# Optimization experiments

Measured on AMD Instinct MI355X. Metric: run time of the kernel, lower is better.

## Reference

```python
import jax, jax.numpy as jnp
import numpy as np

B, T, D, W, H = 64, 512, 768, 255, 8
DH = D // H

def layernorm(x, g, b, eps=1e-5):
    m = jnp.mean(x, axis=-1, keepdims=True)
    v = jnp.mean((x - m) ** 2, axis=-1, keepdims=True)
    return (x - m) * jax.lax.rsqrt(v + eps) * g + b

def setup_inputs() -> dict:
    key = jax.random.key(0)
    ks = list(jax.random.split(key, 12))
    p = lambda k, shape, s=0.02: (jax.random.normal(k, shape, jnp.float32) * s)
    # words_ids: -100 at CLS/SEP, each word spans 2 subtokens -> 255 words/row
    wi = np.full((B, T), -100, dtype=np.int32)
    pos = np.arange(1, T - 1)
    wi[:, 1:T - 1] = (pos - 1) // 2
    return {
        'output_bert': jax.random.normal(ks[0], (B, T, D), jnp.float32),
        'words_ids': jnp.asarray(wi),
        'Wq': p(ks[1], (D, D)), 'bq': jnp.zeros((D,), jnp.float32),
        'Wk': p(ks[2], (D, D)), 'bk': jnp.zeros((D,), jnp.float32),
        'Wv': p(ks[3], (D, D)), 'bv': jnp.zeros((D,), jnp.float32),
        'Wo': p(ks[4], (D, D)), 'bo': jnp.zeros((D,), jnp.float32),
        'ln1_g': jnp.ones((D,), jnp.float32), 'ln1_b': jnp.zeros((D,), jnp.float32),
        'W1f': p(ks[5], (D, 4 * D)), 'b1f': jnp.zeros((4 * D,), jnp.float32),
        'W2f': p(ks[6], (4 * D, D)), 'b2f': jnp.zeros((D,), jnp.float32),
        'ln2_g': jnp.ones((D,), jnp.float32), 'ln2_b': jnp.zeros((D,), jnp.float32),
        'ng': jnp.ones((D,), jnp.float32), 'nb': jnp.zeros((D,), jnp.float32),
        'lin_w': p(ks[7], (D, 2)), 'lin_b': jnp.zeros((2,), jnp.float32),
    }

def reference(output_bert, words_ids, Wq, bq, Wk, bk, Wv, bv, Wo, bo,
              ln1_g, ln1_b, W1f, b1f, W2f, b2f, ln2_g, ln2_b, ng, nb, lin_w, lin_b):
    Bsz = output_bert.shape[0]
    # --- first-subtoken gather: first token position of each word id ---
    hits = words_ids[:, None, :] == jnp.arange(W)[None, :, None]   # [B, W, T]
    first_idx = jnp.argmax(hits, axis=-1)                           # [B, W]
    feat = jnp.take_along_axis(output_bert, first_idx[..., None], axis=1)  # [B, W, D]
    # --- transformer encoder layer (post-norm, relu FFN) ---
    q = (feat @ Wq + bq).reshape(Bsz, W, H, DH)
    k = (feat @ Wk + bk).reshape(Bsz, W, H, DH)
    v = (feat @ Wv + bv).reshape(Bsz, W, H, DH)
    scores = jnp.einsum('bqhd,bkhd->bhqk', q, k) * (1.0 / np.sqrt(DH))
    attn = jax.nn.softmax(scores, axis=-1)
    ctx = jnp.einsum('bhqk,bkhd->bqhd', attn, v).reshape(Bsz, W, D)
    x = layernorm(feat + ctx @ Wo + bo, ln1_g, ln1_b)
    ff = jax.nn.relu(x @ W1f + b1f) @ W2f + b2f
    x = layernorm(x + ff, ln2_g, ln2_b)
    # --- final LayerNorm + Linear + softmax + argmax path ---
    x = layernorm(x, ng, nb)
    logits = x @ lin_w + lin_b
    ner_prob = jax.nn.softmax(logits, axis=-1)
    path = jnp.argmax(ner_prob, axis=-1)
    return ner_prob, path
```

## Files before the change

### kernel.cpp

```cpp
#include <hip/hip_runtime.h>
#include <cmath>

#define Bsz 64
#define Tt  512
#define Dd  768
#define Wn  255
#define Hh  8
#define DHd 96
#define NROWS (Bsz*Wn)

typedef _Float16 half_t;
typedef _Float16 f16x8 __attribute__((ext_vector_type(8)));
typedef _Float16 f16x4 __attribute__((ext_vector_type(4)));
typedef float f32x4 __attribute__((ext_vector_type(4)));

#define OFF_QKV_H 0
#define OFF_QKV_L 1769472
#define OFF_WO_H 3538944
#define OFF_WO_L 4128768
#define OFF_W1_H 4718592
#define OFF_W1_L 7077888
#define OFF_W2_H 9437184
#define OFF_W2_L 11796480
#define SLOTH 25165824
__device__ __align__(16) half_t g_w16[14155776];

__device__ __forceinline__ void gload16(const half_t* g, half_t* l) {
    __builtin_amdgcn_global_load_lds((const __attribute__((address_space(1))) void*)g,
                                     (__attribute__((address_space(3))) void*)l, 16, 0, 0);
}


__global__ void k_init_fi(int* fi) {
    int i = blockIdx.x * 256 + threadIdx.x;
    if (i < Bsz * Wn) fi[i] = 0x7fffffff;
}

__global__ void k_scan(const int* __restrict__ wid, int* __restrict__ fi) {
    int i = blockIdx.x * 256 + threadIdx.x;
    if (i >= Bsz * Tt) return;
    int b = i / Tt, t = i % Tt;
    int w = wid[i];
    if (w >= 0 && w < Wn) atomicMin(&fi[b * Wn + w], t);
}

__global__ void k_bcat(const float* __restrict__ bq, const float* __restrict__ bk,
                       const float* __restrict__ bv, float* __restrict__ o) {
    int i = blockIdx.x * 256 + threadIdx.x;
    if (i < 768) o[i] = bq[i];
    else if (i < 1536) o[i] = bk[i - 768];
    else if (i < 2304) o[i] = bv[i - 1536];
}

__global__ void k_gather(const float4* __restrict__ ob, const int* __restrict__ fi,
                         half_t* __restrict__ f16) {
    int i = blockIdx.x * 256 + threadIdx.x;
    if (i >= NROWS * 192) return;
    int r = i / 192, c = i % 192;
    int b = r / Wn;
    int idx = fi[r];
    if (idx == 0x7fffffff) idx = 0;
    float4 v = ob[((size_t)b * Tt + idx) * 192 + c];
    float a0 = v.x * 16.f, a1 = v.y * 16.f, a2 = v.z * 16.f, a3 = v.w * 16.f;
    half_t h0 = (half_t)a0, h1 = (half_t)a1, h2 = (half_t)a2, h3 = (half_t)a3;
    f16x4 hv = {h0, h1, h2, h3};
    f16x4 lv = {(half_t)(a0 - (float)h0), (half_t)(a1 - (float)h1),
                (half_t)(a2 - (float)h2), (half_t)(a3 - (float)h3)};
    size_t off = (size_t)r * 1536 + c * 4;
    *(f16x4*)&f16[off] = hv;
    *(f16x4*)&f16[off + 768] = lv;
}


__global__ void k_wsplit(const float* __restrict__ Wm, int K, int N,
                         size_t off_h, size_t off_l) {
    __shared__ float sm[32][33];
    const int tx = threadIdx.x, ty = threadIdx.y;
    const int n0 = blockIdx.x * 32, k0 = blockIdx.y * 32;
    #pragma unroll
    for (int r = 0; r < 4; ++r)
        sm[ty + r * 8][tx] = Wm[(size_t)(k0 + ty + r * 8) * N + n0 + tx];
    __syncthreads();
    half_t* oh = g_w16 + off_h;
    half_t* ol = g_w16 + off_l;
    #pragma unroll
    for (int r = 0; r < 4; ++r) {
        float v = 64.f * sm[tx][ty + r * 8];
        half_t hi = (half_t)v;
        size_t o = (size_t)(n0 + ty + r * 8) * K + k0 + tx;
        oh[o] = hi;
        ol[o] = (half_t)(v - (float)hi);
    }
}


template<int MODE, int AMODE, int NTILE>
__global__ __launch_bounds__(256, NTILE == 64 ? 3 : 2) void k_gemm16(
    const half_t* __restrict__ Ah, const half_t* __restrict__ Al, int lda,
    size_t boff_h, size_t boff_l,
    const float* __restrict__ bias,
    const void* __restrict__ res,
    void* __restrict__ out0, void* __restrict__ out1,
    int M, int N, int K) {
    constexpr int MI = (NTILE == 128 ? 4 : 2);
    __shared__ half_t sA[2][128 * 32];
    __shared__ half_t sB[2][NTILE * 32];
    const int tid = threadIdx.x;
    const int w = tid >> 6, l = tid & 63;
    int lin = blockIdx.y * gridDim.x + blockIdx.x;
    int rpx = gridDim.y >> 3;
    int j_ = lin >> 3;
    int jr = j_ / gridDim.x;
    int by = (lin & 7) * rpx + jr;
    int bx = j_ - jr * gridDim.x;
    const int row0 = by * 128, col0 = bx * NTILE;
    const half_t* Bh = g_w16 + boff_h;
    const half_t* Bl = g_w16 + boff_l;

    const int srow = l >> 2;
    const int skk  = (l & 3) * 8;
    const int fr = l & 15, qk = (l >> 4) * 8;
    const int mh = (NTILE == 128) ? (w >> 1) * 64 : w * 32;
    const int nh = (NTILE == 128) ? (w & 1) * 64 : 0;

    f32x4 acc[MI][4];
    #pragma unroll
    for (int i = 0; i < MI; ++i)
        #pragma unroll
        for (int j = 0; j < 4; ++j) acc[i][j] = (f32x4){0.f, 0.f, 0.f, 0.f};

    for (int k0 = 0; k0 < K; k0 += 32) {
        #pragma unroll
        for (int t = 0; t < 2; ++t) {
            int r = (w * 2 + t) * 16 + srow;
            int grA = row0 + r; if (grA >= M) grA = M - 1;
            half_t* da  = (half_t*)&sA[0][(w * 2 + t) * 512];
            half_t* da2 = (half_t*)&sA[1][(w * 2 + t) * 512];
            if (AMODE == 1) {
                int b = grA / 255, wl = grA - b * 255;
                int kk = k0 + skk;
                int h = kk / 96, d = kk - h * 96;
                size_t aoff = ((size_t)(b * 8 + h) * 256 + wl) * 192 + d;
                gload16(Ah + aoff, da);
                gload16(Al + aoff, da2);
            } else {
                gload16(Ah + (size_t)grA * lda + k0 + skk, da);
                gload16(Al + (size_t)grA * lda + k0 + skk, da2);
            }
            if (NTILE == 128 || t == 0) {
                int bs = (NTILE == 128) ? (w * 2 + t) : w;
                int grB = col0 + bs * 16 + srow;
                gload16(Bh + (size_t)grB * K + k0 + skk, (half_t*)&sB[0][bs * 512]);
                gload16(Bl + (size_t)grB * K + k0 + skk, (half_t*)&sB[1][bs * 512]);
            }
        }
        __syncthreads();
        f16x8 a0[MI], a1[MI], b0[4], b1[4];
        #pragma unroll
        for (int i = 0; i < MI; ++i) {
            a0[i] = *(const f16x8*)&sA[0][(mh + i * 16 + fr) * 32 + qk];
            a1[i] = *(const f16x8*)&sA[1][(mh + i * 16 + fr) * 32 + qk];
        }
        #pragma unroll
        for (int j = 0; j < 4; ++j) {
            b0[j] = *(const f16x8*)&sB[0][(nh + j * 16 + fr) * 32 + qk];
            b1[j] = *(const f16x8*)&sB[1][(nh + j * 16 + fr) * 32 + qk];
        }
        #pragma unroll
        for (int i = 0; i < MI; ++i)
            #pragma unroll
            for (int j = 0; j < 4; ++j) {
                acc[i][j] = __builtin_amdgcn_mfma_f32_16x16x32_f16(a0[i], b0[j], acc[i][j], 0, 0, 0);
                acc[i][j] = __builtin_amdgcn_mfma_f32_16x16x32_f16(a0[i], b1[j], acc[i][j], 0, 0, 0);
                acc[i][j] = __builtin_amdgcn_mfma_f32_16x16x32_f16(a1[i], b0[j], acc[i][j], 0, 0, 0);
            }
        __syncthreads();
    }

    const float dsc = 1.0f / 1024.0f;
    #pragma unroll
    for (int i = 0; i < MI; ++i) {
        #pragma unroll
        for (int r = 0; r < 4; ++r) {
            int row = row0 + mh + i * 16 + ((l >> 4) << 2) + r;
            if (row >= M) continue;
            #pragma unroll
            for (int j = 0; j < 4; ++j) {
                int col = col0 + nh + j * 16 + (l & 15);
                float vv = acc[i][j][r] * dsc + bias[col];
                if (MODE == 5) {
                    int b = row / 255, wl = row - b * 255;
                    int part = col / 768;
                    int cc = col - part * 768;
                    int h = cc / 96, d = cc - h * 96;
                    float t16 = vv * 16.f;
                    half_t hi = (half_t)t16;
                    half_t lo = (half_t)(t16 - (float)hi);
                    half_t* dst = (half_t*)out0 + (size_t)part * SLOTH;
                    size_t o = ((size_t)(b * 8 + h) * 256 + wl) * 192 + d;
                    dst[o] = hi; dst[o + 96] = lo;
                } else if (MODE == 1) {
                    const half_t* rp = (const half_t*)res;
                    vv += ((float)rp[(size_t)row * 1536 + col] +
                           (float)rp[(size_t)row * 1536 + 768 + col]) * 0.0625f;
                    ((float*)out0)[(size_t)row * N + col] = vv;
                } else if (MODE == 2) {
                    vv = fmaxf(vv, 0.f);
                    float t16 = vv * 16.f;
                    half_t hi = (half_t)t16;
                    ((half_t*)out0)[(size_t)row * N + col] = hi;
                    ((half_t*)out1)[(size_t)row * N + col] = (half_t)(t16 - (float)hi);
                } else {
                    vv += ((const float*)res)[(size_t)row * N + col];
                    ((float*)out0)[(size_t)row * N + col] = vv;
                }
            }
        }
    }
}


__global__ __launch_bounds__(256, 2) void k_attn2(half_t* __restrict__ qc,
                                                  const half_t* __restrict__ kk16,
                                                  const half_t* __restrict__ vv16) {
    __shared__ half_t sK[64][200];
    __shared__ half_t sVT[192][72];
    __shared__ float  sP[4][16][68];
    const int tid = threadIdx.x;
    const int w = tid >> 6, l = tid & 63;
    const int lr = l & 15, lc = l >> 4;
    const size_t base = (size_t)blockIdx.x * 49152;
    const float ssc = 0.10206207261596575f / 256.0f;

    for (int pass = 0; pass < 2; ++pass) {
        f32x4 O[2][6];
        float mrow[2][4], lrow[2][4];
        #pragma unroll
        for (int qs = 0; qs < 2; ++qs) {
            #pragma unroll
            for (int dn = 0; dn < 6; ++dn) O[qs][dn] = (f32x4){0.f, 0.f, 0.f, 0.f};
            #pragma unroll
            for (int r = 0; r < 4; ++r) { mrow[qs][r] = -3e38f; lrow[qs][r] = 0.f; }
        }
        for (int kt = 0; kt < 4; ++kt) {
            __syncthreads();
            #pragma unroll
            for (int c = 0; c < 6; ++c) {
                int ch = w + c * 4;
                *(f16x8*)&sK[l][ch * 8] =
                    *(const f16x8*)(kk16 + base + (size_t)(kt * 64 + l) * 192 + ch * 8);
            }
            #pragma unroll
            for (int c = 0; c < 6; ++c) {
                int ch = w + c * 4;
                f16x8 vv = *(const f16x8*)(vv16 + base + (size_t)(kt * 64 + l) * 192 + ch * 8);
                #pragma unroll
                for (int j = 0; j < 8; ++j) sVT[ch * 8 + j][l] = vv[j];
            }
            __syncthreads();
            #pragma unroll
            for (int qs = 0; qs < 2; ++qs) {
                const int qrow0 = (pass * 2 + qs) * 64 + w * 16;
                f16x8 qf0[3], qf1[3];
                #pragma unroll
                for (int s = 0; s < 3; ++s) {
                    qf0[s] = *(const f16x8*)(qc + base + (size_t)(qrow0 + lr) * 192 + s * 32 + lc * 8);
                    qf1[s] = *(const f16x8*)(qc + base + (size_t)(qrow0 + lr) * 192 + 96 + s * 32 + lc * 8);
                }
                f32x4 sacc[4];
                #pragma unroll
                for (int nt = 0; nt < 4; ++nt) sacc[nt] = (f32x4){0.f, 0.f, 0.f, 0.f};
                #pragma unroll
                for (int s = 0; s < 3; ++s)
                    #pragma unroll
                    for (int nt = 0; nt < 4; ++nt) {
                        f16x8 kh = *(const f16x8*)&sK[nt * 16 + lr][s * 32 + lc * 8];
                        f16x8 klo = *(const f16x8*)&sK[nt * 16 + lr][96 + s * 32 + lc * 8];
                        sacc[nt] = __builtin_amdgcn_mfma_f32_16x16x32_f16(qf0[s], kh, sacc[nt], 0, 0, 0);
                        sacc[nt] = __builtin_amdgcn_mfma_f32_16x16x32_f16(qf0[s], klo, sacc[nt], 0, 0, 0);
                        sacc[nt] = __builtin_amdgcn_mfma_f32_16x16x32_f16(qf1[s], kh, sacc[nt], 0, 0, 0);
                    }
                float sv[4][4], mx[4] = {-3e38f, -3e38f, -3e38f, -3e38f};
                #pragma unroll
                for (int nt = 0; nt < 4; ++nt) {
                    int key = kt * 64 + nt * 16 + lr;
                    #pragma unroll
                    for (int r = 0; r < 4; ++r) {
                        float s_ = sacc[nt][r] * ssc;
                        if (key >= 255) s_ = -3e38f;
                        sv[nt][r] = s_;
                        mx[r] = fmaxf(mx[r], s_);
                    }
                }
                #pragma unroll
                for (int r = 0; r < 4; ++r) {
                    mx[r] = fmaxf(mx[r], __shfl_xor(mx[r], 1));
                    mx[r] = fmaxf(mx[r], __shfl_xor(mx[r], 2));
                    mx[r] = fmaxf(mx[r], __shfl_xor(mx[r], 4));
                    mx[r] = fmaxf(mx[r], __shfl_xor(mx[r], 8));
                }
                float alpha[4], rsum[4];
                #pragma unroll
                for (int r = 0; r < 4; ++r) {
                    float mn = fmaxf(mrow[qs][r], mx[r]);
                    alpha[r] = __expf(mrow[qs][r] - mn);
                    mrow[qs][r] = mn;
                    rsum[r] = 0.f;
                }
                float pv[4][4];
                #pragma unroll
                for (int nt = 0; nt < 4; ++nt)
                    #pragma unroll
                    for (int r = 0; r < 4; ++r) {
                        float p = __expf(sv[nt][r] - mrow[qs][r]);
                        pv[nt][r] = p;
                        rsum[r] += p;
                    }
                #pragma unroll
                for (int r = 0; r < 4; ++r) {
                    rsum[r] += __shfl_xor(rsum[r], 1);
                    rsum[r] += __shfl_xor(rsum[r], 2);
                    rsum[r] += __shfl_xor(rsum[r], 4);
                    rsum[r] += __shfl_xor(rsum[r], 8);
                    lrow[qs][r] = lrow[qs][r] * alpha[r] + rsum[r];
                }
                #pragma unroll
                for (int dn = 0; dn < 6; ++dn)
                    #pragma unroll
                    for (int r = 0; r < 4; ++r) O[qs][dn][r] *= alpha[r];
                #pragma unroll
                for (int nt = 0; nt < 4; ++nt)
                    #pragma unroll
                    for (int r = 0; r < 4; ++r)
                        sP[w][lc * 4 + r][nt * 16 + lr] = pv[nt][r];
                #pragma unroll
                for (int ks = 0; ks < 2; ++ks) {
                    const float* pp = &sP[w][lr][ks * 32 + lc * 8];
                    f16x8 ph, pl;
                    #pragma unroll
                    for (int j = 0; j < 8; ++j) {
                        float p = pp[j];
                        half_t h_ = (half_t)p;
                        ph[j] = h_;
                        pl[j] = (half_t)(p - (float)h_);
                    }
                    #pragma unroll
                    for (int dn = 0; dn < 6; ++dn) {
                        f16x8 vh = *(const f16x8*)&sVT[dn * 16 + lr][ks * 32 + lc * 8];
                        f16x8 vl = *(const f16x8*)&sVT[96 + dn * 16 + lr][ks * 32 + lc * 8];
                        O[qs][dn] = __builtin_amdgcn_mfma_f32_16x16x32_f16(ph, vh, O[qs][dn], 0, 0, 0);
                        O[qs][dn] = __builtin_amdgcn_mfma_f32_16x16x32_f16(ph, vl, O[qs][dn], 0, 0, 0);
                        O[qs][dn] = __builtin_amdgcn_mfma_f32_16x16x32_f16(pl, vh, O[qs][dn], 0, 0, 0);
                    }
                }
            }
        }
        #pragma unroll
        for (int qs = 0; qs < 2; ++qs) {
            const int qrow0 = (pass * 2 + qs) * 64 + w * 16;
            #pragma unroll
            for (int r = 0; r < 4; ++r) {
                int qrow = qrow0 + lc * 4 + r;
                if (qrow >= Wn) continue;
                float inv = 1.0f / lrow[qs][r];
                #pragma unroll
                for (int dn = 0; dn < 6; ++dn) {
                    float val = O[qs][dn][r] * inv;
                    half_t hi = (half_t)val;
                    half_t lo = (half_t)(val - (float)hi);
                    size_t o = base + (size_t)qrow * 192 + dn * 16 + lr;
                    qc[o] = hi;
                    qc[o + 96] = lo;
                }
            }
        }
    }
}


template<int SPLIT>
__global__ __launch_bounds__(256) void k_ln(const float* __restrict__ X, const float* __restrict__ g,
                                            const float* __restrict__ bt, float* __restrict__ Y,
                                            half_t* __restrict__ Y16) {
    const int r = blockIdx.x, tid = threadIdx.x;
    __shared__ float red[256];
    const float* x = X + (size_t)r * Dd;
    float x0 = x[tid], x1 = x[tid + 256], x2 = x[tid + 512];
    red[tid] = x0 + x1 + x2; __syncthreads();
    for (int s = 128; s > 0; s >>= 1) { if (tid < s) red[tid] += red[tid + s]; __syncthreads(); }
    float mean = red[0] * (1.0f / 768.0f);
    __syncthreads();
    float d0 = x0 - mean, d1 = x1 - mean, d2 = x2 - mean;
    red[tid] = d0 * d0 + d1 * d1 + d2 * d2; __syncthreads();
    for (int s = 128; s > 0; s >>= 1) { if (tid < s) red[tid] += red[tid + s]; __syncthreads(); }
    float rs = rsqrtf(red[0] * (1.0f / 768.0f) + 1e-5f);
    float* y = Y + (size_t)r * Dd;
    float y0 = d0 * rs * g[tid]       + bt[tid];
    float y1 = d1 * rs * g[tid + 256] + bt[tid + 256];
    float y2 = d2 * rs * g[tid + 512] + bt[tid + 512];
    y[tid] = y0; y[tid + 256] = y1; y[tid + 512] = y2;
    if (SPLIT) {
        half_t* h = Y16 + (size_t)r * 1536;
        float t0 = y0 * 16.f, t1 = y1 * 16.f, t2 = y2 * 16.f;
        half_t h0 = (half_t)t0, h1 = (half_t)t1, h2 = (half_t)t2;
        h[tid] = h0; h[tid + 256] = h1; h[tid + 512] = h2;
        h[768 + tid] = (half_t)(t0 - (float)h0);
        h[768 + tid + 256] = (half_t)(t1 - (float)h1);
        h[768 + tid + 512] = (half_t)(t2 - (float)h2);
    }
}


__global__ __launch_bounds__(256) void k_final(const float* __restrict__ X, const float* __restrict__ g,
                                               const float* __restrict__ bt, const float* __restrict__ lw,
                                               const float* __restrict__ lb, float* __restrict__ out) {
    const int r = blockIdx.x, tid = threadIdx.x;
    __shared__ float red[256];
    const float* x = X + (size_t)r * Dd;
    float x0 = x[tid], x1 = x[tid + 256], x2 = x[tid + 512];
    red[tid] = x0 + x1 + x2; __syncthreads();
    for (int s = 128; s > 0; s >>= 1) { if (tid < s) red[tid] += red[tid + s]; __syncthreads(); }
    float mean = red[0] * (1.0f / 768.0f);
    __syncthreads();
    float d0 = x0 - mean, d1 = x1 - mean, d2 = x2 - mean;
    red[tid] = d0 * d0 + d1 * d1 + d2 * d2; __syncthreads();
    for (int s = 128; s > 0; s >>= 1) { if (tid < s) red[tid] += red[tid + s]; __syncthreads(); }
    float rs = rsqrtf(red[0] * (1.0f / 768.0f) + 1e-5f);
    __syncthreads();
    float n0 = d0 * rs * g[tid]       + bt[tid];
    float n1 = d1 * rs * g[tid + 256] + bt[tid + 256];
    float n2 = d2 * rs * g[tid + 512] + bt[tid + 512];
    float l0 = n0 * lw[2 * tid]     + n1 * lw[2 * (tid + 256)]     + n2 * lw[2 * (tid + 512)];
    float l1 = n0 * lw[2 * tid + 1] + n1 * lw[2 * (tid + 256) + 1] + n2 * lw[2 * (tid + 512) + 1];
    red[tid] = l0; __syncthreads();
    for (int s = 128; s > 0; s >>= 1) { if (tid < s) red[tid] += red[tid + s]; __syncthreads(); }
    l0 = red[0]; __syncthreads();
    red[tid] = l1; __syncthreads();
    for (int s = 128; s > 0; s >>= 1) { if (tid < s) red[tid] += red[tid + s]; __syncthreads(); }
    l1 = red[0];
    if (tid == 0) {
        l0 += lb[0]; l1 += lb[1];
        float m = fmaxf(l0, l1);
        float e0 = expf(l0 - m), e1 = expf(l1 - m);
        float inv = 1.0f / (e0 + e1);
        out[2 * r] = e0 * inv;
        out[2 * r + 1] = e1 * inv;
        out[2 * NROWS + r] = (l1 > l0) ? 1.0f : 0.0f;
    }
}


extern "C" void kernel_launch(void* const* d_in, const int* in_sizes, int n_in,
                              void* d_out, int out_size, void* d_ws, size_t ws_size,
                              hipStream_t stream) {
    const float* ob  = (const float*)d_in[0];
    const int*   wid = (const int*)d_in[1];
    const float* Wq  = (const float*)d_in[2];  const float* bq  = (const float*)d_in[3];
    const float* Wk  = (const float*)d_in[4];  const float* bk  = (const float*)d_in[5];
    const float* Wv  = (const float*)d_in[6];  const float* bv  = (const float*)d_in[7];
    const float* Wo  = (const float*)d_in[8];  const float* bo  = (const float*)d_in[9];
    const float* g1  = (const float*)d_in[10]; const float* b1  = (const float*)d_in[11];
    const float* W1f = (const float*)d_in[12]; const float* b1f = (const float*)d_in[13];
    const float* W2f = (const float*)d_in[14]; const float* b2f = (const float*)d_in[15];
    const float* g2  = (const float*)d_in[16]; const float* b2  = (const float*)d_in[17];
    const float* ng  = (const float*)d_in[18]; const float* nb  = (const float*)d_in[19];
    const float* lw  = (const float*)d_in[20]; const float* lb  = (const float*)d_in[21];
    float* out = (float*)d_out;

    char* ws = (char*)d_ws;
    const size_t MB = 1u << 20;
    const size_t SLOT = 48 * MB;
    int* fi = (int*)ws;
    float* bcat = (float*)(ws + 262144);
    char* S1 = ws + MB;
    char* S2 = S1 + SLOT;
    char* S3 = S2 + SLOT;
    char* S4 = S3 + SLOT;

    half_t* feat16 = (half_t*)S1;
    half_t* q16    = (half_t*)S2;
    half_t* k16    = (half_t*)S3;
    half_t* v16    = (half_t*)S4;
    float*  t1     = (float*)S3;
    float*  xbuf   = (float*)S4;
    half_t* x16    = (half_t*)S2;
    half_t* ffh_h  = (half_t*)S1;
    half_t* ffh_l  = (half_t*)S3;
    float*  t2     = (float*)S2;
    float*  x2     = (float*)S4;

    k_wsplit<<<dim3(24, 24), dim3(32, 8), 0, stream>>>(Wq, 768, 768, 0, 1769472);
    k_wsplit<<<dim3(24, 24), dim3(32, 8), 0, stream>>>(Wk, 768, 768, 589824, 2359296);
    k_wsplit<<<dim3(24, 24), dim3(32, 8), 0, stream>>>(Wv, 768, 768, 1179648, 2949120);
    k_wsplit<<<dim3(24, 24), dim3(32, 8), 0, stream>>>(Wo, 768, 768, OFF_WO_H, OFF_WO_L);
    k_wsplit<<<dim3(96, 24), dim3(32, 8), 0, stream>>>(W1f, 768, 3072, OFF_W1_H, OFF_W1_L);
    k_wsplit<<<dim3(24, 96), dim3(32, 8), 0, stream>>>(W2f, 3072, 768, OFF_W2_H, OFF_W2_L);
    k_bcat<<<9, 256, 0, stream>>>(bq, bk, bv, bcat);

    k_init_fi<<<(Bsz * Wn + 255) / 256, 256, 0, stream>>>(fi);
    k_scan<<<(Bsz * Tt) / 256, 256, 0, stream>>>(wid, fi);
    k_gather<<<(NROWS * 192 + 255) / 256, 256, 0, stream>>>((const float4*)ob, fi, feat16);

    k_gemm16<5, 0, 128><<<dim3(18, 128), 256, 0, stream>>>(
        feat16, feat16 + 768, 1536, OFF_QKV_H, OFF_QKV_L,
        bcat, nullptr, q16, nullptr, NROWS, 2304, Dd);

    k_attn2<<<Bsz * Hh, 256, 0, stream>>>(q16, k16, v16);

    k_gemm16<1, 1, 128><<<dim3(6, 128), 256, 0, stream>>>(
        q16, q16 + 96, 0, OFF_WO_H, OFF_WO_L,
        bo, feat16, t1, nullptr, NROWS, Dd, Dd);
    k_ln<1><<<NROWS, 256, 0, stream>>>(t1, g1, b1, xbuf, x16);

    for (int c = 0; c < 2; ++c) {
        const int r0 = c * 8160, mc = 8160;
        k_gemm16<2, 0, 128><<<dim3(24, 64), 256, 0, stream>>>(
            x16 + (size_t)r0 * 1536, x16 + (size_t)r0 * 1536 + 768, 1536,
            OFF_W1_H, OFF_W1_L, b1f, nullptr, ffh_h, ffh_l, mc, 3072, Dd);
        k_gemm16<3, 0, 64><<<dim3(12, 64), 256, 0, stream>>>(
            ffh_h, ffh_l, 3072, OFF_W2_H, OFF_W2_L, b2f, xbuf + (size_t)r0 * Dd,
            t2 + (size_t)r0 * Dd, nullptr, mc, Dd, 3072);
    }

    k_ln<0><<<NROWS, 256, 0, stream>>>(t2, g2, b2, x2, nullptr);
    k_final<<<NROWS, 256, 0, stream>>>(x2, ng, nb, lw, lb, out);
}
```

Baseline: 1.144 ms.

## Replace split-fp16 GEMMs with 256x256 pipelined kernel over concatenated K segments

Replaces the 128-wide double-buffered GEMM with a 512-thread 256x256 tile kernel. The split-precision hi/lo products become one long K loop over a pre-concatenated [hi|hi|lo] weight layout, so each iteration issues two MFMAs instead of three separate accumulations. The kernel uses XOR-swizzled LDS, split-phase prefetch with explicit vmcnt waits, and s_setprio around MFMA bursts. The FFN is restructured into three hidden-dimension chunks whose W2 outputs accumulate in place into xbuf. This targets larger data reuse and better overlap of loads with compute, but it raises register pressure and leaves partial tiles for M=16320 and N=768.

```diff
diff --git a/kernel.cpp b/kernel.cpp
--- a/kernel.cpp
+++ b/kernel.cpp
@@ -14,16 +14,12 @@
 typedef _Float16 f16x4 __attribute__((ext_vector_type(4)));
 typedef float f32x4 __attribute__((ext_vector_type(4)));
 
-#define OFF_QKV_H 0
-#define OFF_QKV_L 1769472
-#define OFF_WO_H 3538944
-#define OFF_WO_L 4128768
-#define OFF_W1_H 4718592
-#define OFF_W1_L 7077888
-#define OFF_W2_H 9437184
-#define OFF_W2_L 11796480
+#define OFF_QKV 0
+#define OFF_WO  5308416
+#define OFF_W1  7077888
+#define OFF_W2  14155776
 #define SLOTH 25165824
-__device__ __align__(16) half_t g_w16[14155776];
+__device__ __align__(16) half_t g_w16[21233664];
 
 __device__ __forceinline__ void gload16(const half_t* g, half_t* l) {
     __builtin_amdgcn_global_load_lds((const __attribute__((address_space(1))) void*)g,
@@ -73,7 +69,7 @@
 
 
 __global__ void k_wsplit(const float* __restrict__ Wm, int K, int N,
-                         size_t off_h, size_t off_l) {
+                         size_t obase, int Kseg, size_t cstride) {
     __shared__ float sm[32][33];
     const int tx = threadIdx.x, ty = threadIdx.y;
     const int n0 = blockIdx.x * 32, k0 = blockIdx.y * 32;
@@ -81,124 +77,195 @@
     for (int r = 0; r < 4; ++r)
         sm[ty + r * 8][tx] = Wm[(size_t)(k0 + ty + r * 8) * N + n0 + tx];
     __syncthreads();
-    half_t* oh = g_w16 + off_h;
-    half_t* ol = g_w16 + off_l;
     #pragma unroll
     for (int r = 0; r < 4; ++r) {
         float v = 64.f * sm[tx][ty + r * 8];
         half_t hi = (half_t)v;
-        size_t o = (size_t)(n0 + ty + r * 8) * K + k0 + tx;
-        oh[o] = hi;
-        ol[o] = (half_t)(v - (float)hi);
-    }
-}
-
-
-template<int MODE, int AMODE, int NTILE>
-__global__ __launch_bounds__(256, NTILE == 64 ? 3 : 2) void k_gemm16(
+        half_t lo = (half_t)(v - (float)hi);
+        int k = k0 + tx;
+        int n = n0 + ty + r * 8;
+        int c = k / Kseg, kk = k - c * Kseg;
+        half_t* o = g_w16 + obase + (size_t)c * cstride + (size_t)n * (3 * Kseg) + kk;
+        o[0] = hi; o[Kseg] = hi; o[2 * Kseg] = lo;
+    }
+}
+
+
+__device__ __forceinline__ void stage_b(const half_t* B, int Kp3, int col0,
+                                        int t, int c, half_t* dst, int tid) {
+    int gc = col0 + c * 64 + (tid >> 3);
+    int sj = (tid & 7) ^ ((tid >> 3) & 7);
+    gload16(B + (size_t)gc * Kp3 + (size_t)t * 64 + sj * 8,
+            dst + 16384 + c * 4096 + (tid >> 6) * 512);
+}
+
+__device__ __forceinline__ void stage_a0(const half_t* Ap, int lda, int row0, int M,
+                                         int kk, int c, half_t* dst, int tid) {
+    int gr = row0 + c * 64 + (tid >> 3); if (gr > M - 1) gr = M - 1;
+    int sj = (tid & 7) ^ ((tid >> 3) & 7);
+    gload16(Ap + (size_t)gr * lda + kk + sj * 8, dst + c * 4096 + (tid >> 6) * 512);
+}
+
+__device__ __forceinline__ void stage_a1(const half_t* qcb, int row0, int M,
+                                         int kk, int soff, int c, half_t* dst, int tid) {
+    int gr = row0 + c * 64 + (tid >> 3); if (gr > M - 1) gr = M - 1;
+    int sj = (tid & 7) ^ ((tid >> 3) & 7);
+    int k = kk + sj * 8;
+    int h = k / 96, d = k - h * 96;
+    int b = gr / 255, wl = gr - b * 255;
+    gload16(qcb + ((size_t)(b * 8 + h) * 256 + wl) * 192 + d + soff,
+            dst + c * 4096 + (tid >> 6) * 512);
+}
+
+template<int MODE, int AMODE>
+__global__ __launch_bounds__(512, 2) void k_gemm256(
     const half_t* __restrict__ Ah, const half_t* __restrict__ Al, int lda,
-    size_t boff_h, size_t boff_l,
-    const float* __restrict__ bias,
-    const void* __restrict__ res,
-    void* __restrict__ out0, void* __restrict__ out1,
+    size_t boff, const float* __restrict__ bias,
+    const void* res, void* out0, void* out1,
     int M, int N, int K) {
-    constexpr int MI = (NTILE == 128 ? 4 : 2);
-    __shared__ half_t sA[2][128 * 32];
-    __shared__ half_t sB[2][NTILE * 32];
+    __shared__ half_t sm[2][32768];
     const int tid = threadIdx.x;
     const int w = tid >> 6, l = tid & 63;
+    const int wm = w >> 2, wn = w & 3;
+    const int fr = l & 15, q4 = l >> 4;
+    const int ck0 = (q4 * 8) ^ ((fr & 7) << 3);
+    const int ck1 = ck0 ^ 32;
+    const half_t* Bsrc = g_w16 + boff;
+    const int Kp3 = 3 * K, NT = Kp3 >> 6;
+
     int lin = blockIdx.y * gridDim.x + blockIdx.x;
-    int rpx = gridDim.y >> 3;
-    int j_ = lin >> 3;
-    int jr = j_ / gridDim.x;
-    int by = (lin & 7) * rpx + jr;
-    int bx = j_ - jr * gridDim.x;
-    const int row0 = by * 128, col0 = bx * NTILE;
-    const half_t* Bh = g_w16 + boff_h;
-    const half_t* Bl = g_w16 + boff_l;
-
-    const int srow = l >> 2;
-    const int skk  = (l & 3) * 8;
-    const int fr = l & 15, qk = (l >> 4) * 8;
-    const int mh = (NTILE == 128) ? (w >> 1) * 64 : w * 32;
-    const int nh = (NTILE == 128) ? (w & 1) * 64 : 0;
-
-    f32x4 acc[MI][4];
+    int nwg = gridDim.x * gridDim.y;
+    int wg = (lin & 7) * (nwg >> 3) + (lin >> 3);
+    int by = wg / gridDim.x, bx = wg - by * gridDim.x;
+    const int row0 = by * 256, col0 = bx * 256;
+
+    f32x4 acc[8][4];
     #pragma unroll
-    for (int i = 0; i < MI; ++i)
-        #pragma unroll
-        for (int j = 0; j < 4; ++j) acc[i][j] = (f32x4){0.f, 0.f, 0.f, 0.f};
-
-    for (int k0 = 0; k0 < K; k0 += 32) {
-        #pragma unroll
-        for (int t = 0; t < 2; ++t) {
-            int r = (w * 2 + t) * 16 + srow;
-            int grA = row0 + r; if (grA >= M) grA = M - 1;
-            half_t* da  = (half_t*)&sA[0][(w * 2 + t) * 512];
-            half_t* da2 = (half_t*)&sA[1][(w * 2 + t) * 512];
-            if (AMODE == 1) {
-                int b = grA / 255, wl = grA - b * 255;
-                int kk = k0 + skk;
-                int h = kk / 96, d = kk - h * 96;
-                size_t aoff = ((size_t)(b * 8 + h) * 256 + wl) * 192 + d;
-                gload16(Ah + aoff, da);
-                gload16(Al + aoff, da2);
+    for (int m = 0; m < 8; ++m)
+        #pragma unroll
+        for (int n = 0; n < 4; ++n) acc[m][n] = (f32x4){0.f, 0.f, 0.f, 0.f};
+
+    {
+        half_t* d0 = &sm[0][0];
+        stage_b(Bsrc, Kp3, col0, 0, 0, d0, tid);
+        stage_b(Bsrc, Kp3, col0, 0, 1, d0, tid);
+        stage_b(Bsrc, Kp3, col0, 0, 2, d0, tid);
+        stage_b(Bsrc, Kp3, col0, 0, 3, d0, tid);
+        if (AMODE == 0) {
+            stage_a0(Ah, lda, row0, M, 0, 0, d0, tid);
+            stage_a0(Ah, lda, row0, M, 0, 2, d0, tid);
+            stage_a0(Ah, lda, row0, M, 0, 1, d0, tid);
+            stage_a0(Ah, lda, row0, M, 0, 3, d0, tid);
+        } else {
+            stage_a1(Ah, row0, M, 0, 0, 0, d0, tid);
+            stage_a1(Ah, row0, M, 0, 0, 2, d0, tid);
+            stage_a1(Ah, row0, M, 0, 0, 1, d0, tid);
+            stage_a1(Ah, row0, M, 0, 0, 3, d0, tid);
+        }
+    }
+    asm volatile("s_waitcnt vmcnt(2)" ::: "memory");
+    __builtin_amdgcn_s_barrier();
+    asm volatile("" ::: "memory");
+
+    for (int t = 0; t < NT; ++t) {
+        const int p = t & 1;
+        half_t* nxtb = &sm[p ^ 1][0];
+        const half_t* pA = &sm[p][0] + wm * 8192;
+        const half_t* pB = &sm[p][0] + 16384 + wn * 4096;
+        const bool pf = (t + 1) < NT;
+        const int kn = (t + 1) << 6;
+        const int seg = (kn >= 2 * K) ? 2 : ((kn >= K) ? 1 : 0);
+        const int kkn = kn - seg * K;
+        const half_t* An = (seg == 1) ? Al : Ah;
+        const int soff = (seg == 1) ? 96 : 0;
+
+        f16x8 b0[4], b1[4], a0[4], a1[4];
+        #pragma unroll
+        for (int n = 0; n < 4; ++n) {
+            b0[n] = *(const f16x8*)&pB[n * 1024 + fr * 64 + ck0];
+            b1[n] = *(const f16x8*)&pB[n * 1024 + fr * 64 + ck1];
+        }
+        #pragma unroll
+        for (int m = 0; m < 4; ++m) {
+            a0[m] = *(const f16x8*)&pA[m * 1024 + fr * 64 + ck0];
+            a1[m] = *(const f16x8*)&pA[m * 1024 + fr * 64 + ck1];
+        }
+        if (pf) {
+            stage_b(Bsrc, Kp3, col0, t + 1, 0, nxtb, tid);
+            stage_b(Bsrc, Kp3, col0, t + 1, 1, nxtb, tid);
+            stage_b(Bsrc, Kp3, col0, t + 1, 2, nxtb, tid);
+            stage_b(Bsrc, Kp3, col0, t + 1, 3, nxtb, tid);
+        }
+        __builtin_amdgcn_s_setprio(1);
+        #pragma unroll
+        for (int m = 0; m < 4; ++m)
+            #pragma unroll
+            for (int n = 0; n < 4; ++n) {
+                acc[m][n] = __builtin_amdgcn_mfma_f32_16x16x32_f16(a0[m], b0[n], acc[m][n], 0, 0, 0);
+                acc[m][n] = __builtin_amdgcn_mfma_f32_16x16x32_f16(a1[m], b1[n], acc[m][n], 0, 0, 0);
+            }
+        __builtin_amdgcn_s_setprio(0);
+        if (pf) asm volatile("s_waitcnt vmcnt(4)" ::: "memory");
+        else    asm volatile("s_waitcnt vmcnt(0)" ::: "memory");
+        __builtin_amdgcn_s_barrier();
+        asm volatile("" ::: "memory");
+
+        #pragma unroll
+        for (int m = 0; m < 4; ++m) {
+            a0[m] = *(const f16x8*)&pA[4096 + m * 1024 + fr * 64 + ck0];
+            a1[m] = *(const f16x8*)&pA[4096 + m * 1024 + fr * 64 + ck1];
+        }
+        if (pf) {
+            if (AMODE == 0) {
+                stage_a0(An, lda, row0, M, kkn, 0, nxtb, tid);
+                stage_a0(An, lda, row0, M, kkn, 2, nxtb, tid);
+                stage_a0(An, lda, row0, M, kkn, 1, nxtb, tid);
+                stage_a0(An, lda, row0, M, kkn, 3, nxtb, tid);
             } else {
-                gload16(Ah + (size_t)grA * lda + k0 + skk, da);
-                gload16(Al + (size_t)grA * lda + k0 + skk, da2);
-            }
-            if (NTILE == 128 || t == 0) {
-                int bs = (NTILE == 128) ? (w * 2 + t) : w;
-                int grB = col0 + bs * 16 + srow;
-                gload16(Bh + (size_t)grB * K + k0 + skk, (half_t*)&sB[0][bs * 512]);
-                gload16(Bl + (size_t)grB * K + k0 + skk, (half_t*)&sB[1][bs * 512]);
-            }
-        }
-        __syncthreads();
-        f16x8 a0[MI], a1[MI], b0[4], b1[4];
-        #pragma unroll
-        for (int i = 0; i < MI; ++i) {
-            a0[i] = *(const f16x8*)&sA[0][(mh + i * 16 + fr) * 32 + qk];
-            a1[i] = *(const f16x8*)&sA[1][(mh + i * 16 + fr) * 32 + qk];
-        }
-        #pragma unroll
-        for (int j = 0; j < 4; ++j) {
-            b0[j] = *(const f16x8*)&sB[0][(nh + j * 16 + fr) * 32 + qk];
-            b1[j] = *(const f16x8*)&sB[1][(nh + j * 16 + fr) * 32 + qk];
-        }
-        #pragma unroll
-        for (int i = 0; i < MI; ++i)
-            #pragma unroll
-            for (int j = 0; j < 4; ++j) {
-                acc[i][j] = __builtin_amdgcn_mfma_f32_16x16x32_f16(a0[i], b0[j], acc[i][j], 0, 0, 0);
-                acc[i][j] = __builtin_amdgcn_mfma_f32_16x16x32_f16(a0[i], b1[j], acc[i][j], 0, 0, 0);
-                acc[i][j] = __builtin_amdgcn_mfma_f32_16x16x32_f16(a1[i], b0[j], acc[i][j], 0, 0, 0);
-            }
-        __syncthreads();
+                stage_a1(Ah, row0, M, kkn, soff, 0, nxtb, tid);
+                stage_a1(Ah, row0, M, kkn, soff, 2, nxtb, tid);
+                stage_a1(Ah, row0, M, kkn, soff, 1, nxtb, tid);
+                stage_a1(Ah, row0, M, kkn, soff, 3, nxtb, tid);
+            }
+        }
+        __builtin_amdgcn_s_setprio(1);
+        #pragma unroll
+        for (int m = 0; m < 4; ++m)
+            #pragma unroll
+            for (int n = 0; n < 4; ++n) {
+                acc[4 + m][n] = __builtin_amdgcn_mfma_f32_16x16x32_f16(a0[m], b0[n], acc[4 + m][n], 0, 0, 0);
+                acc[4 + m][n] = __builtin_amdgcn_mfma_f32_16x16x32_f16(a1[m], b1[n], acc[4 + m][n], 0, 0, 0);
+            }
+        __builtin_amdgcn_s_setprio(0);
+        if (pf) {
+            asm volatile("s_waitcnt vmcnt(2)" ::: "memory");
+            __builtin_amdgcn_s_barrier();
+            asm volatile("" ::: "memory");
+        }
     }
 
     const float dsc = 1.0f / 1024.0f;
     #pragma unroll
-    for (int i = 0; i < MI; ++i) {
+    for (int m = 0; m < 8; ++m) {
         #pragma unroll
         for (int r = 0; r < 4; ++r) {
-            int row = row0 + mh + i * 16 + ((l >> 4) << 2) + r;
+            const int row = row0 + wm * 128 + m * 16 + q4 * 4 + r;
             if (row >= M) continue;
             #pragma unroll
-            for (int j = 0; j < 4; ++j) {
-                int col = col0 + nh + j * 16 + (l & 15);
-                float vv = acc[i][j][r] * dsc + bias[col];
+            for (int n = 0; n < 4; ++n) {
+                const int col = col0 + wn * 64 + n * 16 + fr;
+                float vv = acc[m][n][r] * dsc;
+                if (MODE != 4) vv += bias[col];
                 if (MODE == 5) {
+                    int part = col / 768, cc = col - part * 768;
+                    int h = cc / 96, d = cc - h * 96;
                     int b = row / 255, wl = row - b * 255;
-                    int part = col / 768;
-                    int cc = col - part * 768;
-                    int h = cc / 96, d = cc - h * 96;
                     float t16 = vv * 16.f;
                     half_t hi = (half_t)t16;
                     half_t lo = (half_t)(t16 - (float)hi);
-                    half_t* dst = (half_t*)out0 + (size_t)part * SLOTH;
+                    half_t* dstp = (half_t*)out0 + (size_t)part * SLOTH;
                     size_t o = ((size_t)(b * 8 + h) * 256 + wl) * 192 + d;
-                    dst[o] = hi; dst[o + 96] = lo;
+                    dstp[o] = hi; dstp[o + 96] = lo;
                 } else if (MODE == 1) {
                     const half_t* rp = (const half_t*)res;
                     vv += ((float)rp[(size_t)row * 1536 + col] +
@@ -210,9 +277,12 @@
                     half_t hi = (half_t)t16;
                     ((half_t*)out0)[(size_t)row * N + col] = hi;
                     ((half_t*)out1)[(size_t)row * N + col] = (half_t)(t16 - (float)hi);
-                } else {
+                } else if (MODE == 3) {
                     vv += ((const float*)res)[(size_t)row * N + col];
                     ((float*)out0)[(size_t)row * N + col] = vv;
+                } else {
+                    float* op = (float*)out0 + (size_t)row * N + col;
+                    *op += vv;
                 }
             }
         }
@@ -486,42 +556,42 @@
     half_t* x16    = (half_t*)S2;
     half_t* ffh_h  = (half_t*)S1;
     half_t* ffh_l  = (half_t*)S3;
-    float*  t2     = (float*)S2;
-    float*  x2     = (float*)S4;
-
-    k_wsplit<<<dim3(24, 24), dim3(32, 8), 0, stream>>>(Wq, 768, 768, 0, 1769472);
-    k_wsplit<<<dim3(24, 24), dim3(32, 8), 0, stream>>>(Wk, 768, 768, 589824, 2359296);
-    k_wsplit<<<dim3(24, 24), dim3(32, 8), 0, stream>>>(Wv, 768, 768, 1179648, 2949120);
-    k_wsplit<<<dim3(24, 24), dim3(32, 8), 0, stream>>>(Wo, 768, 768, OFF_WO_H, OFF_WO_L);
-    k_wsplit<<<dim3(96, 24), dim3(32, 8), 0, stream>>>(W1f, 768, 3072, OFF_W1_H, OFF_W1_L);
-    k_wsplit<<<dim3(24, 96), dim3(32, 8), 0, stream>>>(W2f, 3072, 768, OFF_W2_H, OFF_W2_L);
+    float*  x2     = (float*)S2;
+
+    k_wsplit<<<dim3(24, 24), dim3(32, 8), 0, stream>>>(Wq, 768, 768, OFF_QKV,                   768, 0);
+    k_wsplit<<<dim3(24, 24), dim3(32, 8), 0, stream>>>(Wk, 768, 768, OFF_QKV + 768ul * 2304,    768, 0);
+    k_wsplit<<<dim3(24, 24), dim3(32, 8), 0, stream>>>(Wv, 768, 768, OFF_QKV + 1536ul * 2304,   768, 0);
+    k_wsplit<<<dim3(24, 24), dim3(32, 8), 0, stream>>>(Wo, 768, 768, OFF_WO,                    768, 0);
+    k_wsplit<<<dim3(96, 24), dim3(32, 8), 0, stream>>>(W1f, 768, 3072, OFF_W1,                  768, 0);
+    k_wsplit<<<dim3(24, 96), dim3(32, 8), 0, stream>>>(W2f, 3072, 768, OFF_W2,                 1024, 768ul * 3072);
     k_bcat<<<9, 256, 0, stream>>>(bq, bk, bv, bcat);
 
     k_init_fi<<<(Bsz * Wn + 255) / 256, 256, 0, stream>>>(fi);
     k_scan<<<(Bsz * Tt) / 256, 256, 0, stream>>>(wid, fi);
     k_gather<<<(NROWS * 192 + 255) / 256, 256, 0, stream>>>((const float4*)ob, fi, feat16);
 
-    k_gemm16<5, 0, 128><<<dim3(18, 128), 256, 0, stream>>>(
-        feat16, feat16 + 768, 1536, OFF_QKV_H, OFF_QKV_L,
-        bcat, nullptr, q16, nullptr, NROWS, 2304, Dd);
+    k_gemm256<5, 0><<<dim3(9, 64), 512, 0, stream>>>(
+        feat16, feat16 + 768, 1536, OFF_QKV, bcat, nullptr, q16, nullptr, NROWS, 2304, 768);
 
     k_attn2<<<Bsz * Hh, 256, 0, stream>>>(q16, k16, v16);
 
-    k_gemm16<1, 1, 128><<<dim3(6, 128), 256, 0, stream>>>(
-        q16, q16 + 96, 0, OFF_WO_H, OFF_WO_L,
-        bo, feat16, t1, nullptr, NROWS, Dd, Dd);
+    k_gemm256<1, 1><<<dim3(3, 64), 512, 0, stream>>>(
+        q16, q16 + 96, 0, OFF_WO, bo, feat16, t1, nullptr, NROWS, 768, 768);
     k_ln<1><<<NROWS, 256, 0, stream>>>(t1, g1, b1, xbuf, x16);
 
-    for (int c = 0; c < 2; ++c) {
-        const int r0 = c * 8160, mc = 8160;
-        k_gemm16<2, 0, 128><<<dim3(24, 64), 256, 0, stream>>>(
-            x16 + (size_t)r0 * 1536, x16 + (size_t)r0 * 1536 + 768, 1536,
-            OFF_W1_H, OFF_W1_L, b1f, nullptr, ffh_h, ffh_l, mc, 3072, Dd);
-        k_gemm16<3, 0, 64><<<dim3(12, 64), 256, 0, stream>>>(
-            ffh_h, ffh_l, 3072, OFF_W2_H, OFF_W2_L, b2f, xbuf + (size_t)r0 * Dd,
-            t2 + (size_t)r0 * Dd, nullptr, mc, Dd, 3072);
-    }
-
-    k_ln<0><<<NROWS, 256, 0, stream>>>(t2, g2, b2, x2, nullptr);
+    for (int c = 0; c < 3; ++c) {
+        k_gemm256<2, 0><<<dim3(4, 64), 512, 0, stream>>>(
+            x16, x16 + 768, 1536, OFF_W1 + (size_t)c * 1024 * 2304, b1f + c * 1024,
+            nullptr, ffh_h, ffh_l, NROWS, 1024, 768);
+        if (c == 0)
+            k_gemm256<3, 0><<<dim3(3, 64), 512, 0, stream>>>(
+                ffh_h, ffh_l, 1024, OFF_W2, b2f, xbuf, xbuf, nullptr, NROWS, 768, 1024);
+        else
+            k_gemm256<4, 0><<<dim3(3, 64), 512, 0, stream>>>(
+                ffh_h, ffh_l, 1024, OFF_W2 + (size_t)c * 768 * 3072, b2f,
+                nullptr, xbuf, nullptr, NROWS, 768, 1024);
+    }
+
+    k_ln<0><<<NROWS, 256, 0, stream>>>(xbuf, g2, b2, x2, nullptr);
     k_final<<<NROWS, 256, 0, stream>>>(x2, ng, nb, lw, lb, out);
 }
```

Measured after the change: 1.206 ms. 1.05x slower.
